# Kernel optimization log

Measured on AMD Instinct MI355X. Metric: run time of the kernel, lower is better.

## Reference

```python
import jax, jax.numpy as jnp
import numpy as np
from math import sqrt

N, I, H, O = 2048, 16, 32, 32
CUTS = 8
RADIUS = 9.0
GROUPS = 4
EPS = 1e-5


def leaky(x):
    return jnp.where(x >= 0, x, 0.2 * x)


def group_norm(x, gamma, beta):
    # x: (N, C). Torch applies GroupNorm(4, C) on (1, C, N):
    # normalize over (channels-in-group, N) jointly.
    n, c = x.shape
    xt = x.T.reshape(GROUPS, (c // GROUPS) * n)          # (G, C/G * N)
    mu = xt.mean(axis=1, keepdims=True)
    var = xt.var(axis=1, keepdims=True)
    xn = ((xt - mu) / jnp.sqrt(var + EPS)).reshape(c, n)
    return (xn * gamma[:, None] + beta[:, None]).T       # (N, C)


def setup_inputs() -> dict:
    key = jax.random.key(0)
    ks = jax.random.split(key, 20)
    inp = {
        "points": jax.random.normal(ks[0], (N, 3), jnp.float32) * 5.0,
        "nuv": jax.random.normal(ks[1], (N, 3, 3), jnp.float32),
        "features": jax.random.normal(ks[2], (N, I), jnp.float32),
        # net_in: Linear(I,H), Linear(H,H)
        "W_in1": jax.random.normal(ks[3], (H, I), jnp.float32) / np.sqrt(I),
        "b_in1": jax.random.normal(ks[4], (H,), jnp.float32) * 0.01,
        "W_in2": jax.random.normal(ks[5], (H, H), jnp.float32) / np.sqrt(H),
        "b_in2": jax.random.normal(ks[6], (H,), jnp.float32) * 0.01,
        "g_in_w": jnp.ones((H,), jnp.float32),
        "g_in_b": jnp.zeros((H,), jnp.float32),
        # conv: Linear(3, CUTS), Linear(CUTS, H) with custom init
        "A1": jax.random.normal(ks[7], (CUTS, 3), jnp.float32),
        "A2": jax.random.uniform(ks[9], (H, CUTS), jnp.float32,
                                 minval=-1.0 / np.sqrt(CUTS), maxval=1.0 / np.sqrt(CUTS)),
        # net_out: Linear(H,O), Linear(O,O)
        "W_out1": jax.random.normal(ks[11], (O, H), jnp.float32) / np.sqrt(H),
        "b_out1": jax.random.normal(ks[12], (O,), jnp.float32) * 0.01,
        "W_out2": jax.random.normal(ks[13], (O, O), jnp.float32) / np.sqrt(O),
        "b_out2": jax.random.normal(ks[14], (O,), jnp.float32) * 0.01,
        "g_out_w": jnp.ones((O,), jnp.float32),
        "g_out_b": jnp.zeros((O,), jnp.float32),
    }
    inp["B1"] = (jax.random.uniform(ks[8], (CUTS,), jnp.float32)
                 * 0.8 * jnp.sqrt((inp["A1"] ** 2).sum(-1)))
    inp["B2"] = (jax.random.normal(ks[10], (H,), jnp.float32)
                 * 0.5 * jnp.sqrt((inp["A2"] ** 2).sum(-1)))
    return inp


def reference(points, nuv, features,
              W_in1, b_in1, W_in2, b_in2, g_in_w, g_in_b,
              A1, B1, A2, B2,
              W_out1, b_out1, W_out2, b_out2, g_out_w, g_out_b):
    # 1) net_in + GroupNorm on (1, H, N)
    f = leaky(features @ W_in1.T + b_in1)
    f = leaky(f @ W_in2.T + b_in2)
    f = group_norm(f, g_in_w, g_in_b)                    # (N, H)

    # 2) quasi-geodesic all-pairs interaction
    pts = points / (sqrt(2.0) * RADIUS)
    normals = jax.lax.stop_gradient(nuv[:, 0, :])        # (N, 3), detached
    diff = pts[None, :, :] - pts[:, None, :]             # (N, N, 3) = x_j - x_i
    sq_dist = (diff ** 2).sum(-1)                        # (N, N)
    dot_nn = normals @ normals.T                         # (N, N)
    window = jnp.exp(-sq_dist * (2.0 - dot_nn) ** 2)     # (N, N)

    X_ij = jnp.einsum('iac,ijc->ija', nuv, diff)         # (N, N, 3) local coords
    Xc = jax.nn.relu(jnp.einsum('ijk,ck->ijc', X_ij, A1) + B1)   # (N, N, CUTS)
    Xc = jax.nn.relu(jnp.einsum('ijc,hc->ijh', Xc, A2) + B2)     # (N, N, H)

    F_ij = window[:, :, None] * Xc * f[None, :, :]       # (N, N, H)
    f = F_ij.sum(axis=1)                                 # (N, H)

    # 3) net_out + GroupNorm
    f = leaky(f @ W_out1.T + b_out1)
    f = leaky(f @ W_out2.T + b_out2)
    return group_norm(f, g_out_w, g_out_b)               # (N, O)
```

## Files before the change

kernel.cpp:

```cpp
#include <hip/hip_runtime.h>
#include <hip/hip_bf16.h>

#define NPTS   2048
#define IDIM   16
#define HDIM   32
#define CUTSN  8
#define EPSV   1e-5f
#define PSCALE 0.07856742013183862f
#define ICH    16
#define IPK    48

typedef __bf16 bf16x8 __attribute__((ext_vector_type(8)));
typedef float  f32x16 __attribute__((ext_vector_type(16)));

__device__ __forceinline__ float leaky(float x) { return x >= 0.f ? x : 0.2f * x; }

template <int K>
__global__ __launch_bounds__(256) void net2_kernel(
    const float* __restrict__ xin,
    const float* __restrict__ W1, const float* __restrict__ b1,
    const float* __restrict__ W2, const float* __restrict__ b2,
    float* __restrict__ out, float* __restrict__ partials,
    float* __restrict__ zbuf,
    const float* __restrict__ points, const float* __restrict__ nuv,
    const float* __restrict__ A1, const float* __restrict__ B1,
    float* __restrict__ ipack)
{
    const int t = threadIdx.x;
    const int i = blockIdx.x * 256 + t;
    if (zbuf) {
#pragma unroll
        for (int e = 0; e < 8; ++e)
            *(float4*)&zbuf[i * HDIM + e * 4] = make_float4(0.f, 0.f, 0.f, 0.f);
    }
    if (ipack) {
        float* ip = ipack + i * IPK;
#pragma unroll
        for (int c = 0; c < 8; ++c) {
            float m0 = 0.f, m1 = 0.f, m2 = 0.f;
#pragma unroll
            for (int a = 0; a < 3; ++a) {
                const float wA = A1[c * 3 + a];
                m0 = fmaf(wA, nuv[i * 9 + a * 3 + 0], m0);
                m1 = fmaf(wA, nuv[i * 9 + a * 3 + 1], m1);
                m2 = fmaf(wA, nuv[i * 9 + a * 3 + 2], m2);
            }
            *(float4*)&ip[c * 4] = make_float4(m0, m1, m2, B1[c]);
        }
        *(float4*)&ip[32] = make_float4(points[i * 3 + 0] * PSCALE,
                                        points[i * 3 + 1] * PSCALE,
                                        points[i * 3 + 2] * PSCALE,
                                        nuv[i * 9 + 0]);
        *(float4*)&ip[36] = make_float4(nuv[i * 9 + 1], nuv[i * 9 + 2], 0.f, 0.f);
        *(float4*)&ip[40] = make_float4(0.f, 0.f, 0.f, 0.f);
        *(float4*)&ip[44] = make_float4(0.f, 0.f, 0.f, 0.f);
    }

    float x[K];
#pragma unroll
    for (int k = 0; k < K; ++k) x[k] = xin[i * K + k];

    float y[HDIM];
#pragma unroll
    for (int h = 0; h < HDIM; ++h) {
        float v = b1[h];
#pragma unroll
        for (int k = 0; k < K; ++k) v = fmaf(x[k], W1[h * K + k], v);
        y[h] = leaky(v);
    }
    float ps[4]  = {0.f, 0.f, 0.f, 0.f};
    float pss[4] = {0.f, 0.f, 0.f, 0.f};
#pragma unroll
    for (int h = 0; h < HDIM; ++h) {
        float v = b2[h];
#pragma unroll
        for (int k = 0; k < HDIM; ++k) v = fmaf(y[k], W2[h * HDIM + k], v);
        v = leaky(v);
        out[i * HDIM + h] = v;
        const int g = h >> 3;
        ps[g] += v; pss[g] = fmaf(v, v, pss[g]);
    }
#pragma unroll
    for (int off = 32; off; off >>= 1) {
#pragma unroll
        for (int g = 0; g < 4; ++g) {
            ps[g]  += __shfl_down(ps[g],  off, 64);
            pss[g] += __shfl_down(pss[g], off, 64);
        }
    }
    __shared__ float lred[4][8];
    const int wv = t >> 6, ln = t & 63;
    if (ln == 0) {
#pragma unroll
        for (int g = 0; g < 4; ++g) { lred[wv][g] = ps[g]; lred[wv][4 + g] = pss[g]; }
    }
    __syncthreads();
    if (t < 8) {
        const float v = lred[0][t] + lred[1][t] + lred[2][t] + lred[3][t];
        partials[t * 8 + blockIdx.x] = v;
    }
}

__global__ __launch_bounds__(256) void gn_apply_kernel(
    const float* __restrict__ x, const float* __restrict__ partials,
    const float* __restrict__ gw, const float* __restrict__ gb,
    float* __restrict__ out)
{
    const int idx = blockIdx.x * 256 + threadIdx.x;
    const int c = idx & (HDIM - 1);
    const int g = c >> 3;
    float s = 0.f, q = 0.f;
#pragma unroll
    for (int b = 0; b < 8; ++b) {
        s += partials[g * 8 + b];
        q += partials[32 + g * 8 + b];
    }
    const float inv = 1.f / (8.f * NPTS);
    const float mu = s * inv;
    const float rs = rsqrtf(q * inv - mu * mu + EPSV);
    out[idx] = fmaf((x[idx] - mu) * rs, gw[c], gb[c]);
}

__global__ __launch_bounds__(512, 1) void pairwise_kernel(
    const float* __restrict__ points, const float* __restrict__ nuv,
    const float* __restrict__ A2, const float* __restrict__ B2,
    const float* __restrict__ ipack,
    const float* __restrict__ traw, const float* __restrict__ partials,
    const float* __restrict__ gw, const float* __restrict__ gb,
    float* __restrict__ fout)
{
    const int t     = threadIdx.x;
    const int lane  = t & 63;
    const int wave  = __builtin_amdgcn_readfirstlane(t >> 6);
    const int h     = lane & 31;
    const int khalf = lane >> 5;
    const int ibase = blockIdx.y * ICH;
    const int jt0   = blockIdx.x * 256 + wave * 32;

    __shared__ float sacc[ICH][32];
    if (t < ICH * 32) ((float*)sacc)[t] = 0.f;

    const int j = jt0 + h;
    const float pjx = points[j * 3 + 0] * PSCALE;
    const float pjy = points[j * 3 + 1] * PSCALE;
    const float pjz = points[j * 3 + 2] * PSCALE;
    const float njx = nuv[j * 9 + 0], njy = nuv[j * 9 + 1], njz = nuv[j * 9 + 2];

    bf16x8 bfrag;
#pragma unroll
    for (int e = 0; e < 8; ++e) {
        const float bv = (khalf == 0) ? A2[h * 8 + e] : (e == 0 ? B2[h] : 0.f);
        bfrag[e] = (__bf16)bv;
    }

    const int g4 = h >> 3;
    float s = 0.f, q = 0.f;
#pragma unroll
    for (int b = 0; b < 8; ++b) {
        s += partials[g4 * 8 + b];
        q += partials[32 + g4 * 8 + b];
    }
    const float inv = 1.f / (8.f * NPTS);
    const float mu = s * inv;
    const float rs = rsqrtf(q * inv - mu * mu + EPSV);
    const float alpha = rs * gw[h];
    const float gamma = fmaf(-mu, alpha, gb[h]);
    float freg[16];
#pragma unroll
    for (int r = 0; r < 16; ++r) {
        const int jr = (r & 3) + 8 * (r >> 2) + 4 * khalf;
        freg[r] = fmaf(traw[(jt0 + jr) * HDIM + h], alpha, gamma);
    }

    f32x16 czero;
#pragma unroll
    for (int e = 0; e < 16; ++e) czero[e] = 0.f;

    __syncthreads();

#define LOADI(M, G0, G1, il) do {                                             \
        const float4* ip4 = (const float4*)(ipack + (ibase + (il)) * IPK);    \
        M[0] = ip4[0]; M[1] = ip4[1]; M[2] = ip4[2]; M[3] = ip4[3];           \
        M[4] = ip4[4]; M[5] = ip4[5]; M[6] = ip4[6]; M[7] = ip4[7];           \
        G0 = ip4[8]; G1 = ip4[9];                                             \
    } while (0)

#define BODY(M, G0, G1, il) do {                                              \
        const float dx = pjx - G0.x, dy = pjy - G0.y, dz = pjz - G0.z;        \
        const float sq = fmaf(dx, dx, fmaf(dy, dy, dz * dz));                 \
        const float dt = fmaf(G0.w, njx, fmaf(G1.x, njy, G1.y * njz));        \
        const float tt = 2.f - dt;                                            \
        const float wv = __expf(-sq * tt * tt);                               \
        float u[8];                                                           \
        _Pragma("unroll")                                                     \
        for (int c = 0; c < 8; ++c) {                                         \
            const float cut = fmaf(M[c].x, dx, fmaf(M[c].y, dy,               \
                              fmaf(M[c].z, dz, M[c].w)));                     \
            u[c] = wv * fmaxf(cut, 0.f);                                      \
        }                                                                     \
        bf16x8 afrag;                                                         \
        afrag[0] = (__bf16)(khalf == 0 ? u[0] : wv);                          \
        _Pragma("unroll")                                                     \
        for (int e = 1; e < 8; ++e)                                           \
            afrag[e] = (__bf16)(khalf == 0 ? u[e] : 0.f);                     \
        const f32x16 d = __builtin_amdgcn_mfma_f32_32x32x16_bf16(             \
            afrag, bfrag, czero, 0, 0, 0);                                    \
        float p0 = 0.f, p1 = 0.f, p2 = 0.f, p3 = 0.f;                         \
        _Pragma("unroll")                                                     \
        for (int r = 0; r < 16; r += 4) {                                     \
            p0 = fmaf(fmaxf(d[r],     0.f), freg[r],     p0);                 \
            p1 = fmaf(fmaxf(d[r + 1], 0.f), freg[r + 1], p1);                 \
            p2 = fmaf(fmaxf(d[r + 2], 0.f), freg[r + 2], p2);                 \
            p3 = fmaf(fmaxf(d[r + 3], 0.f), freg[r + 3], p3);                 \
        }                                                                     \
        atomicAdd(&sacc[il][h], (p0 + p1) + (p2 + p3));                       \
    } while (0)

    float4 MA[8], MB[8], GA0, GA1, GB0, GB1;
    LOADI(MA, GA0, GA1, 0);
#pragma unroll 1
    for (int ii = 0; ii < ICH; ii += 2) {
        LOADI(MB, GB0, GB1, ii + 1);
        BODY(MA, GA0, GA1, ii);
        if (ii + 2 < ICH) LOADI(MA, GA0, GA1, ii + 2);
        BODY(MB, GB0, GB1, ii + 1);
    }
#undef LOADI
#undef BODY

    __syncthreads();

    {
        const int il0 = t >> 5, h0 = t & 31;
        atomicAdd(&fout[(ibase + il0) * HDIM + h0], sacc[il0][h0]);
    }
}

extern "C" void kernel_launch(void* const* d_in, const int* in_sizes, int n_in,
                              void* d_out, int out_size, void* d_ws, size_t ws_size,
                              hipStream_t stream)
{
    const float* points   = (const float*)d_in[0];
    const float* nuv      = (const float*)d_in[1];
    const float* features = (const float*)d_in[2];
    const float* W_in1    = (const float*)d_in[3];
    const float* b_in1    = (const float*)d_in[4];
    const float* W_in2    = (const float*)d_in[5];
    const float* b_in2    = (const float*)d_in[6];
    const float* g_in_w   = (const float*)d_in[7];
    const float* g_in_b   = (const float*)d_in[8];
    const float* A1       = (const float*)d_in[9];
    const float* A2       = (const float*)d_in[10];
    const float* W_out1   = (const float*)d_in[11];
    const float* b_out1   = (const float*)d_in[12];
    const float* W_out2   = (const float*)d_in[13];
    const float* b_out2   = (const float*)d_in[14];
    const float* g_out_w  = (const float*)d_in[15];
    const float* g_out_b  = (const float*)d_in[16];
    const float* B1       = (const float*)d_in[17];
    const float* B2       = (const float*)d_in[18];

    float* ws    = (float*)d_ws;
    float* t2a   = ws;
    float* t2b   = ws + 65536;
    float* fout  = ws + 131072;
    float* ipack = ws + 196608;
    float* part1 = ws + 294912;
    float* part2 = ws + 294976;
    float* out   = (float*)d_out;

    net2_kernel<IDIM><<<dim3(NPTS / 256), dim3(256), 0, stream>>>(
        features, W_in1, b_in1, W_in2, b_in2, t2a, part1, fout,
        points, nuv, A1, B1, ipack);

    pairwise_kernel<<<dim3(NPTS / 256, NPTS / ICH), dim3(512), 0, stream>>>(
        points, nuv, A2, B2, ipack, t2a, part1, g_in_w, g_in_b, fout);

    net2_kernel<HDIM><<<dim3(NPTS / 256), dim3(256), 0, stream>>>(
        fout, W_out1, b_out1, W_out2, b_out2, t2b, part2, nullptr,
        nullptr, nullptr, nullptr, nullptr, nullptr);
    gn_apply_kernel<<<dim3(NPTS * HDIM / 256), dim3(256), 0, stream>>>(
        t2b, part2, g_out_w, g_out_b, out);
}
```

Measured before the change: 178.7 us.

## Unroll pairwise i-loop with register accumulators and shrink MLP blocks to one wave

The pairwise kernel's double-buffered macro loop is replaced by a fully unrolled 16-iteration loop. Each iteration stores its result in a register array, with a sched_barrier every 8 iterations, and the shared-memory atomics are deferred to the end. This is meant to give the scheduler freedom to overlap loads, exp, and MFMA while cutting LDS atomic latency from the inner loop, at the cost of more registers. The MLP kernels now use 64-thread blocks and 32 blocks, which removes the LDS reduction and barrier and spreads the work over more CUs. The GroupNorm partials layout is widened to match.

Result: slower. 266.4 us (+49.1%).

```diff
diff --git a/kernel.cpp b/kernel.cpp
--- a/kernel.cpp
+++ b/kernel.cpp
@@ -16,7 +16,7 @@
 __device__ __forceinline__ float leaky(float x) { return x >= 0.f ? x : 0.2f * x; }
 
 template <int K>
-__global__ __launch_bounds__(256) void net2_kernel(
+__global__ __launch_bounds__(64) void net2_kernel(
     const float* __restrict__ xin,
     const float* __restrict__ W1, const float* __restrict__ b1,
     const float* __restrict__ W2, const float* __restrict__ b2,
@@ -27,7 +27,7 @@
     float* __restrict__ ipack)
 {
     const int t = threadIdx.x;
-    const int i = blockIdx.x * 256 + t;
+    const int i = blockIdx.x * 64 + t;
     if (zbuf) {
 #pragma unroll
         for (int e = 0; e < 8; ++e)
@@ -88,16 +88,12 @@
             pss[g] += __shfl_down(pss[g], off, 64);
         }
     }
-    __shared__ float lred[4][8];
-    const int wv = t >> 6, ln = t & 63;
-    if (ln == 0) {
-#pragma unroll
-        for (int g = 0; g < 4; ++g) { lred[wv][g] = ps[g]; lred[wv][4 + g] = pss[g]; }
-    }
-    __syncthreads();
-    if (t < 8) {
-        const float v = lred[0][t] + lred[1][t] + lred[2][t] + lred[3][t];
-        partials[t * 8 + blockIdx.x] = v;
+    if (t == 0) {
+#pragma unroll
+        for (int g = 0; g < 4; ++g) {
+            partials[g * 32 + blockIdx.x]       = ps[g];
+            partials[128 + g * 32 + blockIdx.x] = pss[g];
+        }
     }
 }
 
@@ -111,9 +107,9 @@
     const int g = c >> 3;
     float s = 0.f, q = 0.f;
 #pragma unroll
-    for (int b = 0; b < 8; ++b) {
-        s += partials[g * 8 + b];
-        q += partials[32 + g * 8 + b];
+    for (int b = 0; b < 32; ++b) {
+        s += partials[g * 32 + b];
+        q += partials[128 + g * 32 + b];
     }
     const float inv = 1.f / (8.f * NPTS);
     const float mu = s * inv;
@@ -131,14 +127,14 @@
 {
     const int t     = threadIdx.x;
     const int lane  = t & 63;
-    const int wave  = __builtin_amdgcn_readfirstlane(t >> 6);
     const int h     = lane & 31;
     const int khalf = lane >> 5;
     const int ibase = blockIdx.y * ICH;
-    const int jt0   = blockIdx.x * 256 + wave * 32;
+    const int jt0   = blockIdx.x * 256 + (t >> 6) * 32;
 
     __shared__ float sacc[ICH][32];
     if (t < ICH * 32) ((float*)sacc)[t] = 0.f;
+    __syncthreads();
 
     const int j = jt0 + h;
     const float pjx = points[j * 3 + 0] * PSCALE;
@@ -156,9 +152,9 @@
     const int g4 = h >> 3;
     float s = 0.f, q = 0.f;
 #pragma unroll
-    for (int b = 0; b < 8; ++b) {
-        s += partials[g4 * 8 + b];
-        q += partials[32 + g4 * 8 + b];
+    for (int b = 0; b < 32; ++b) {
+        s += partials[g4 * 32 + b];
+        q += partials[128 + g4 * 32 + b];
     }
     const float inv = 1.f / (8.f * NPTS);
     const float mu = s * inv;
@@ -176,58 +172,58 @@
 #pragma unroll
     for (int e = 0; e < 16; ++e) czero[e] = 0.f;
 
-    __syncthreads();
-
-#define LOADI(M, G0, G1, il) do {                                             \
-        const float4* ip4 = (const float4*)(ipack + (ibase + (il)) * IPK);    \
-        M[0] = ip4[0]; M[1] = ip4[1]; M[2] = ip4[2]; M[3] = ip4[3];           \
-        M[4] = ip4[4]; M[5] = ip4[5]; M[6] = ip4[6]; M[7] = ip4[7];           \
-        G0 = ip4[8]; G1 = ip4[9];                                             \
-    } while (0)
-
-#define BODY(M, G0, G1, il) do {                                              \
-        const float dx = pjx - G0.x, dy = pjy - G0.y, dz = pjz - G0.z;        \
-        const float sq = fmaf(dx, dx, fmaf(dy, dy, dz * dz));                 \
-        const float dt = fmaf(G0.w, njx, fmaf(G1.x, njy, G1.y * njz));        \
-        const float tt = 2.f - dt;                                            \
-        const float wv = __expf(-sq * tt * tt);                               \
-        float u[8];                                                           \
-        _Pragma("unroll")                                                     \
-        for (int c = 0; c < 8; ++c) {                                         \
-            const float cut = fmaf(M[c].x, dx, fmaf(M[c].y, dy,               \
-                              fmaf(M[c].z, dz, M[c].w)));                     \
-            u[c] = wv * fmaxf(cut, 0.f);                                      \
-        }                                                                     \
-        bf16x8 afrag;                                                         \
-        afrag[0] = (__bf16)(khalf == 0 ? u[0] : wv);                          \
-        _Pragma("unroll")                                                     \
-        for (int e = 1; e < 8; ++e)                                           \
-            afrag[e] = (__bf16)(khalf == 0 ? u[e] : 0.f);                     \
-        const f32x16 d = __builtin_amdgcn_mfma_f32_32x32x16_bf16(             \
-            afrag, bfrag, czero, 0, 0, 0);                                    \
-        float p0 = 0.f, p1 = 0.f, p2 = 0.f, p3 = 0.f;                         \
-        _Pragma("unroll")                                                     \
-        for (int r = 0; r < 16; r += 4) {                                     \
-            p0 = fmaf(fmaxf(d[r],     0.f), freg[r],     p0);                 \
-            p1 = fmaf(fmaxf(d[r + 1], 0.f), freg[r + 1], p1);                 \
-            p2 = fmaf(fmaxf(d[r + 2], 0.f), freg[r + 2], p2);                 \
-            p3 = fmaf(fmaxf(d[r + 3], 0.f), freg[r + 3], p3);                 \
-        }                                                                     \
-        atomicAdd(&sacc[il][h], (p0 + p1) + (p2 + p3));                       \
-    } while (0)
-
-    float4 MA[8], MB[8], GA0, GA1, GB0, GB1;
-    LOADI(MA, GA0, GA1, 0);
-#pragma unroll 1
-    for (int ii = 0; ii < ICH; ii += 2) {
-        LOADI(MB, GB0, GB1, ii + 1);
-        BODY(MA, GA0, GA1, ii);
-        if (ii + 2 < ICH) LOADI(MA, GA0, GA1, ii + 2);
-        BODY(MB, GB0, GB1, ii + 1);
-    }
-#undef LOADI
-#undef BODY
-
+    float accv[ICH];
+#pragma unroll
+    for (int il = 0; il < ICH; ++il) accv[il] = 0.f;
+
+#pragma unroll
+    for (int il = 0; il < ICH; ++il) {
+        const float4* ip4 = (const float4*)(ipack + (ibase + il) * IPK);
+        const float4 m0 = ip4[0], m1 = ip4[1], m2 = ip4[2], m3 = ip4[3];
+        const float4 m4 = ip4[4], m5 = ip4[5], m6 = ip4[6], m7 = ip4[7];
+        const float4 G0 = ip4[8], G1 = ip4[9];
+
+        const float dx = pjx - G0.x, dy = pjy - G0.y, dz = pjz - G0.z;
+        const float sq = fmaf(dx, dx, fmaf(dy, dy, dz * dz));
+        const float dt = fmaf(G0.w, njx, fmaf(G1.x, njy, G1.y * njz));
+        const float tt = 2.f - dt;
+        const float wv = __expf(-sq * tt * tt);
+
+        float u[8];
+        u[0] = wv * fmaxf(fmaf(m0.x, dx, fmaf(m0.y, dy, fmaf(m0.z, dz, m0.w))), 0.f);
+        u[1] = wv * fmaxf(fmaf(m1.x, dx, fmaf(m1.y, dy, fmaf(m1.z, dz, m1.w))), 0.f);
+        u[2] = wv * fmaxf(fmaf(m2.x, dx, fmaf(m2.y, dy, fmaf(m2.z, dz, m2.w))), 0.f);
+        u[3] = wv * fmaxf(fmaf(m3.x, dx, fmaf(m3.y, dy, fmaf(m3.z, dz, m3.w))), 0.f);
+        u[4] = wv * fmaxf(fmaf(m4.x, dx, fmaf(m4.y, dy, fmaf(m4.z, dz, m4.w))), 0.f);
+        u[5] = wv * fmaxf(fmaf(m5.x, dx, fmaf(m5.y, dy, fmaf(m5.z, dz, m5.w))), 0.f);
+        u[6] = wv * fmaxf(fmaf(m6.x, dx, fmaf(m6.y, dy, fmaf(m6.z, dz, m6.w))), 0.f);
+        u[7] = wv * fmaxf(fmaf(m7.x, dx, fmaf(m7.y, dy, fmaf(m7.z, dz, m7.w))), 0.f);
+
+        bf16x8 afrag;
+        afrag[0] = (__bf16)(khalf == 0 ? u[0] : wv);
+#pragma unroll
+        for (int e = 1; e < 8; ++e)
+            afrag[e] = (__bf16)(khalf == 0 ? u[e] : 0.f);
+
+        const f32x16 d = __builtin_amdgcn_mfma_f32_32x32x16_bf16(
+            afrag, bfrag, czero, 0, 0, 0);
+
+        float p0 = 0.f, p1 = 0.f, p2 = 0.f, p3 = 0.f;
+#pragma unroll
+        for (int r = 0; r < 16; r += 4) {
+            p0 = fmaf(fmaxf(d[r],     0.f), freg[r],     p0);
+            p1 = fmaf(fmaxf(d[r + 1], 0.f), freg[r + 1], p1);
+            p2 = fmaf(fmaxf(d[r + 2], 0.f), freg[r + 2], p2);
+            p3 = fmaf(fmaxf(d[r + 3], 0.f), freg[r + 3], p3);
+        }
+        accv[il] = (p0 + p1) + (p2 + p3);
+
+        if ((il & 7) == 7) __builtin_amdgcn_sched_barrier(0);
+    }
+
+#pragma unroll
+    for (int il = 0; il < ICH; ++il)
+        atomicAdd(&sacc[il][h], accv[il]);
     __syncthreads();
 
     {
@@ -266,17 +262,17 @@
     float* fout  = ws + 131072;
     float* ipack = ws + 196608;
     float* part1 = ws + 294912;
-    float* part2 = ws + 294976;
+    float* part2 = ws + 295168;
     float* out   = (float*)d_out;
 
-    net2_kernel<IDIM><<<dim3(NPTS / 256), dim3(256), 0, stream>>>(
+    net2_kernel<IDIM><<<dim3(NPTS / 64), dim3(64), 0, stream>>>(
         features, W_in1, b_in1, W_in2, b_in2, t2a, part1, fout,
         points, nuv, A1, B1, ipack);
 
     pairwise_kernel<<<dim3(NPTS / 256, NPTS / ICH), dim3(512), 0, stream>>>(
         points, nuv, A2, B2, ipack, t2a, part1, g_in_w, g_in_b, fout);
 
-    net2_kernel<HDIM><<<dim3(NPTS / 256), dim3(256), 0, stream>>>(
+    net2_kernel<HDIM><<<dim3(NPTS / 64), dim3(64), 0, stream>>>(
         fout, W_out1, b_out1, W_out2, b_out2, t2b, part2, nullptr,
         nullptr, nullptr, nullptr, nullptr, nullptr);
     gn_apply_kernel<<<dim3(NPTS * HDIM / 256), dim3(256), 0, stream>>>(
```
